# Performance work log

Measured on AMD Instinct MI355X. Metric: run time of the kernel, lower is better.

The kernel has to match this reference:

```python
import jax, jax.numpy as jnp
import numpy as np

NEG_INF = -9e15  # matches torch's -9000000000000000.0 fill
ALPHA = 0.2      # LeakyReLU negative slope


def setup_inputs() -> dict:
    key = jax.random.key(0)
    k1, k2, k3, k4 = jax.random.split(key, 4)
    B, F, N, T, C = 16, 128, 256, 64, 64
    h = jax.random.normal(k1, (B, F, N, T), dtype=jnp.float32)
    adj = jax.random.randint(k2, (B, N, N), 0, 2, dtype=jnp.int32)
    W = jax.random.normal(k3, (B, F, C), dtype=jnp.float32)
    a = jax.random.normal(k4, (B, 2 * C, 1), dtype=jnp.float32)
    return {"h": h, "adj": adj, "W": W, "a": a}


def reference(h, adj, W, a):
    # Wh: (B, C, N, T)
    Wh = jnp.einsum('bfnt,bfc->bcnt', h, W)
    C = W.shape[-1]
    # The original builds the O(N^2) pairwise concat then contracts with a.
    # Equivalently: e[b,i,j,t] = leakyrelu(a1.Wh[:, i] + a2.Wh[:, j])
    a1 = a[:, :C, 0]   # (B, C)
    a2 = a[:, C:, 0]   # (B, C)
    f = jnp.einsum('bcnt,bc->bnt', Wh, a1)  # (B, N, T)
    g = jnp.einsum('bcnt,bc->bnt', Wh, a2)  # (B, N, T)
    e = jax.nn.leaky_relu(f[:, :, None, :] + g[:, None, :, :], negative_slope=ALPHA)  # (B,N,N,T)
    mask = adj[:, :, :, None] > 0  # (B, N, N, 1) broadcast over T
    e = jnp.where(mask, e, NEG_INF)
    attention = jax.nn.softmax(e, axis=2)  # softmax over neighbor index m
    # dropout = 0.0 (eval-mode reference), so skipped
    h_prime = jnp.einsum('bnmt,bcmt->bcnt', attention, Wh)
    return jax.nn.elu(h_prime)  # concat=True branch
```

## Files before the change

### kernel.cpp

```cpp
#include <hip/hip_runtime.h>

#define B_ 16
#define F_ 128
#define N_ 256
#define T_ 64
#define C_ 64
#define ALPHA_ 0.2f
#define L2E_ 1.4426950408889634f

typedef short bf16x8 __attribute__((ext_vector_type(8)));
typedef float f32x4 __attribute__((ext_vector_type(4)));

__device__ __forceinline__ unsigned short f2bf(float x){
  unsigned int u = __float_as_uint(x);
  unsigned int r = u + 0x7FFFu + ((u >> 16) & 1u);
  return (unsigned short)(r >> 16);
}
__device__ __forceinline__ unsigned pk2(float a, float b){
  return ((unsigned)f2bf(b) << 16) | (unsigned)f2bf(a);
}
__device__ __forceinline__ unsigned sbit(unsigned w, int j){
  return (unsigned)(((int)(w << (31 - j))) >> 31);
}
__device__ __forceinline__ int swzT(int c){
  return ((c & 7) ^ ((c >> 3) & 7)) << 4;
}

__global__ void k_u(const float* __restrict__ W, const float* __restrict__ a,
                    float* __restrict__ u){
  int b = blockIdx.x, f = threadIdx.x;
  const float* Wb = W + (b*F_ + f)*C_;
  const float* ab = a + b*2*C_;
  float s1 = 0.f, s2 = 0.f;
#pragma unroll 8
  for (int c = 0; c < C_; ++c){
    float w = Wb[c];
    s1 = fmaf(w, ab[c], s1);
    s2 = fmaf(w, ab[C_ + c], s2);
  }
  u[b*F_ + f] = s1;
  u[B_*F_ + b*F_ + f] = s2;
}

__global__ __launch_bounds__(256, 4) void k_whm(const float* __restrict__ h,
    const float* __restrict__ W, const float* __restrict__ u,
    const int* __restrict__ adj,
    unsigned short* __restrict__ wht, float* __restrict__ fvec,
    float* __restrict__ gvec, unsigned* __restrict__ amask){
  __shared__ uint4 hT4[1024];
  __shared__ uint4 wT4[1024];
  __shared__ float fpart[4][T_];
  __shared__ float gpart[4][T_];
  char* hT = (char*)hT4;
  char* wT = (char*)wT4;

  int bid = blockIdx.x;
  int tid = threadIdx.x, w = tid >> 6, l = tid & 63;

  if (bid >= B_*N_){
    int blk = bid - B_*N_;
    int b = blk >> 2, r0 = (blk & 3)*64;
    const int* ab = adj + ((size_t)b*N_ + r0 + w*16)*N_;
    unsigned* om = amask + ((size_t)b*N_ + r0 + w*16)*8;
    for (int r = 0; r < 16; ++r){
      unsigned long long m0 = __ballot(ab[r*N_ +       l] > 0);
      unsigned long long m1 = __ballot(ab[r*N_ +  64 + l] > 0);
      unsigned long long m2 = __ballot(ab[r*N_ + 128 + l] > 0);
      unsigned long long m3 = __ballot(ab[r*N_ + 192 + l] > 0);
      if (l == 0){
        *(uint4*)(om + r*8)     = make_uint4((unsigned)m0, (unsigned)(m0>>32),
                                             (unsigned)m1, (unsigned)(m1>>32));
        *(uint4*)(om + r*8 + 4) = make_uint4((unsigned)m2, (unsigned)(m2>>32),
                                             (unsigned)m3, (unsigned)(m3>>32));
      }
    }
    return;
  }

  int b = bid >> 8, n = bid & 255;
  const float* hg = h + (size_t)b*F_*N_*T_ + n*T_;
  const float* Wg = W + b*F_*C_;
  const float* u1 = u + b*F_;
  const float* u2 = u + B_*F_ + b*F_;

  float sf = 0.f, sg = 0.f;
#pragma unroll
  for (int p = 0; p < 4; ++p){
    int f0 = p*32 + w*8;
    float v[8], wv[8];
#pragma unroll
    for (int j = 0; j < 8; ++j){
      v[j]  = hg[(size_t)(f0+j)*(N_*T_) + l];
      wv[j] = Wg[(f0+j)*C_ + l];
      sf = fmaf(v[j], u1[f0+j], sf);
      sg = fmaf(v[j], u2[f0+j], sg);
    }
    uint4 ph = make_uint4(pk2(v[0],v[1]),  pk2(v[2],v[3]),  pk2(v[4],v[5]),  pk2(v[6],v[7]));
    uint4 pw = make_uint4(pk2(wv[0],wv[1]),pk2(wv[2],wv[3]),pk2(wv[4],wv[5]),pk2(wv[6],wv[7]));
    *(uint4*)(hT + ((l*256 + f0*2) ^ ((l & 7) << 4))) = ph;
    *(uint4*)(wT + ((l*256 + f0*2) ^ ((l & 7) << 4))) = pw;
  }
  fpart[w][l] = sf;
  gpart[w][l] = sg;
  __syncthreads();

  if (tid < T_){
    float f_ = (fpart[0][tid] + fpart[1][tid]) + (fpart[2][tid] + fpart[3][tid]);
    float g_ = (gpart[0][tid] + gpart[1][tid]) + (gpart[2][tid] + gpart[3][tid]);
    fvec[(b*N_ + n)*T_ + tid] = f_ * L2E_;
    gvec[(b*N_ + n)*T_ + tid] = g_ * L2E_;
  }

  int li = l & 15, g_ = l >> 4;
  bf16x8 afr[4];
#pragma unroll
  for (int ch = 0; ch < 4; ++ch){
    int c = w*16 + li;
    afr[ch] = *(bf16x8*)(wT + ((c*256 + (ch*32 + g_*8)*2) ^ ((c & 7) << 4)));
  }
  f32x4 acc[4];
#pragma unroll
  for (int tt = 0; tt < 4; ++tt) acc[tt] = (f32x4){0.f,0.f,0.f,0.f};
#pragma unroll
  for (int tt = 0; tt < 4; ++tt){
#pragma unroll
    for (int ch = 0; ch < 4; ++ch){
      int t = tt*16 + li;
      bf16x8 bfr = *(bf16x8*)(hT + ((t*256 + (ch*32 + g_*8)*2) ^ ((t & 7) << 4)));
      acc[tt] = __builtin_amdgcn_mfma_f32_16x16x32_bf16(afr[ch], bfr, acc[tt], 0, 0, 0);
    }
  }

  __syncthreads();
  char* outT = hT;
#pragma unroll
  for (int tt = 0; tt < 4; ++tt){
    int t = tt*16 + li;
    int c0 = w*16 + g_*4;
    unsigned q0 = pk2(acc[tt][0], acc[tt][1]);
    unsigned q1 = pk2(acc[tt][2], acc[tt][3]);
    *(uint2*)(outT + ((t*128 + c0*2) ^ ((t & 7) << 4))) = make_uint2(q0, q1);
  }
  __syncthreads();
  unsigned short* wb = wht + (size_t)b*T_*N_*C_ + n*C_;
#pragma unroll
  for (int k = 0; k < 2; ++k){
    int idx = tid + k*256;
    int t = idx >> 3, c8 = idx & 7;
    uint4 vq = *(const uint4*)(outT + t*128 + ((c8 ^ (t & 7)) << 4));
    *(uint4*)(wb + (size_t)t*(N_*C_) + c8*8) = vq;
  }
}

__global__ __launch_bounds__(256, 4) void k_attn(
    unsigned short* wht,
    const unsigned* __restrict__ amask,
    const float* __restrict__ fvec,
    const float* __restrict__ gvec){
  __shared__ uint4 whsT4[2048];
  __shared__ float gs[N_];
  __shared__ float fs[N_];
  __shared__ float invs[N_];
  char* dstT = (char*)whsT4;

  int bid = blockIdx.x;
  int b = bid >> 6, t = bid & 63;
  int tid = threadIdx.x, w = tid >> 6, l = tid & 63;
  int li = l & 15, g_ = l >> 4;

  gs[tid] = gvec[(b*N_ + tid)*T_ + t];
  fs[tid] = fvec[(b*N_ + tid)*T_ + t];

  uint4 mlo[4], mhi[4];
#pragma unroll
  for (int mt = 0; mt < 4; ++mt){
    int n = w*64 + mt*16 + li;
    const uint4* mp = (const uint4*)(amask + ((size_t)b*N_ + n)*8);
    mlo[mt] = mp[0];
    mhi[mt] = mp[1];
  }
  unsigned pkl[4], pkh[4];
  unsigned selA = 0x0C0C0000u | ((unsigned)(g_ + 4) << 8) | (unsigned)g_;
#pragma unroll
  for (int mt = 0; mt < 4; ++mt){
    unsigned t0 = __builtin_amdgcn_perm(mlo[mt].y, mlo[mt].x, selA);
    unsigned t1 = __builtin_amdgcn_perm(mlo[mt].w, mlo[mt].z, selA);
    pkl[mt] = __builtin_amdgcn_perm(t1, t0, 0x05040100u);
    unsigned t2 = __builtin_amdgcn_perm(mhi[mt].y, mhi[mt].x, selA);
    unsigned t3 = __builtin_amdgcn_perm(mhi[mt].w, mhi[mt].z, selA);
    pkh[mt] = __builtin_amdgcn_perm(t3, t2, 0x05040100u);
  }

  const char* src = (const char*)(wht + (size_t)(b*T_ + t)*(N_*C_));
  uint4 ra[4], rb[4];
#pragma unroll
  for (int i = 0; i < 4; ++i){
    int q2 = tid + i*256;
    int m = (q2 >> 3)*2, c0 = (q2 & 7)*8;
    ra[i] = *(const uint4*)(src + m*128 + c0*2);
    rb[i] = *(const uint4*)(src + (m+1)*128 + c0*2);
  }

  asm volatile("s_waitcnt lgkmcnt(0)" ::: "memory");
  __builtin_amdgcn_sched_barrier(0);
  __builtin_amdgcn_s_barrier();

  float fl2[4];
#pragma unroll
  for (int mt = 0; mt < 4; ++mt) fl2[mt] = fs[w*64 + mt*16 + li];

  float mg[4] = {0.f, 0.f, 0.f, 0.f};
#pragma unroll 1
  for (int ch = 0; ch < 8; ++ch){
    const float* gq = &gs[ch*32 + g_*8];
    float4 ga = *(const float4*)gq;
    float4 gb = *(const float4*)(gq + 4);
    float gg[8] = {ga.x, ga.y, ga.z, ga.w, gb.x, gb.y, gb.z, gb.w};
    int sh = (ch & 3)*8;
#pragma unroll
    for (int mt = 0; mt < 4; ++mt){
      unsigned wsh = ((ch & 4) ? pkh[mt] : pkl[mt]) >> sh;
      float cd[8];
#pragma unroll
      for (int j = 0; j < 8; ++j)
        cd[j] = __uint_as_float(__float_as_uint(gg[j]) & sbit(wsh, j));
      float m01 = fmaxf(cd[0], cd[1]), m23 = fmaxf(cd[2], cd[3]);
      float m45 = fmaxf(cd[4], cd[5]), m67 = fmaxf(cd[6], cd[7]);
      mg[mt] = fmaxf(mg[mt], fmaxf(fmaxf(m01, m23), fmaxf(m45, m67)));
    }
  }
  float fme[4], fme2[4];
#pragma unroll
  for (int mt = 0; mt < 4; ++mt){
    float v = mg[mt];
    v = fmaxf(v, __shfl_xor(v, 16));
    v = fmaxf(v, __shfl_xor(v, 32));
    float em = fl2[mt] + v;
    float M  = fmaxf(em, ALPHA_*em);
    fme[mt]  = fl2[mt] - M;
    fme2[mt] = fmaf(fl2[mt], ALPHA_, -M);
  }

#pragma unroll
  for (int i = 0; i < 4; ++i){
    int q2 = tid + i*256;
    int m = (q2 >> 3)*2, c0 = (q2 & 7)*8;
    unsigned va[4] = {ra[i].x, ra[i].y, ra[i].z, ra[i].w};
    unsigned vb[4] = {rb[i].x, rb[i].y, rb[i].z, rb[i].w};
#pragma unroll
    for (int k = 0; k < 4; ++k){
      int c = c0 + 2*k;
      unsigned lo = __builtin_amdgcn_perm(vb[k], va[k], 0x05040100u);
      unsigned hi = __builtin_amdgcn_perm(vb[k], va[k], 0x07060302u);
      *(unsigned*)(dstT + ((c*512 + m*2)     ^ swzT(c)))   = lo;
      *(unsigned*)(dstT + (((c+1)*512 + m*2) ^ swzT(c+1))) = hi;
    }
  }
  __syncthreads();

  f32x4 acc[4][4];
#pragma unroll
  for (int mt = 0; mt < 4; ++mt)
#pragma unroll
    for (int nt = 0; nt < 4; ++nt)
      acc[mt][nt] = (f32x4){0.f, 0.f, 0.f, 0.f};
  float s0[4] = {0.f,0.f,0.f,0.f}, s1[4] = {0.f,0.f,0.f,0.f};

#pragma unroll 2
  for (int ch = 0; ch < 8; ++ch){
    bf16x8 bfr[4];
#pragma unroll
    for (int nt = 0; nt < 4; ++nt){
      int c = nt*16 + li;
      bfr[nt] = *(bf16x8*)(dstT + ((c*512 + (ch*32 + g_*8)*2) ^ swzT(c)));
    }
    const float* gq = &gs[ch*32 + g_*8];
    float4 ga = *(const float4*)gq;
    float4 gb = *(const float4*)(gq + 4);
    float gg[8] = {ga.x, ga.y, ga.z, ga.w, gb.x, gb.y, gb.z, gb.w};
    int sh = (ch & 3)*8;
#pragma unroll
    for (int mt = 0; mt < 4; ++mt){
      unsigned wsh = ((ch & 4) ? pkh[mt] : pkl[mt]) >> sh;
      float wv[8];
#pragma unroll
      for (int j = 0; j < 8; ++j){
        float d1 = gg[j] + fme[mt];
        float d2 = fmaf(gg[j], ALPHA_, fme2[mt]);
        float p  = exp2f(fmaxf(d1, d2));
        float v  = __uint_as_float(__float_as_uint(p) & sbit(wsh, j));
        if (j < 4) s0[mt] += v; else s1[mt] += v;
        wv[j] = v;
      }
      unsigned q0, q1, q2_, q3;
      asm("v_cvt_pk_bf16_f32 %0, %1, %2" : "=v"(q0)  : "v"(wv[0]), "v"(wv[1]));
      asm("v_cvt_pk_bf16_f32 %0, %1, %2" : "=v"(q1)  : "v"(wv[2]), "v"(wv[3]));
      asm("v_cvt_pk_bf16_f32 %0, %1, %2" : "=v"(q2_) : "v"(wv[4]), "v"(wv[5]));
      asm("v_cvt_pk_bf16_f32 %0, %1, %2" : "=v"(q3)  : "v"(wv[6]), "v"(wv[7]));
      union { unsigned u[4]; bf16x8 v; } afu;
      afu.u[0] = q0; afu.u[1] = q1; afu.u[2] = q2_; afu.u[3] = q3;
#pragma unroll
      for (int nt = 0; nt < 4; ++nt)
        acc[mt][nt] = __builtin_amdgcn_mfma_f32_16x16x32_bf16(afu.v, bfr[nt], acc[mt][nt], 0, 0, 0);
    }
  }

#pragma unroll
  for (int mt = 0; mt < 4; ++mt){
    float s = s0[mt] + s1[mt];
    s += __shfl_xor(s, 16);
    s += __shfl_xor(s, 32);
    if (g_ == 0) invs[w*64 + mt*16 + li] = 1.0f / s;
  }

  unsigned short* ob = wht + (size_t)(b*T_ + t)*(N_*C_);
#pragma unroll
  for (int mt = 0; mt < 4; ++mt){
#pragma unroll
    for (int reg = 0; reg < 4; ++reg){
      int nloc = w*64 + mt*16 + g_*4 + reg;
      float inv = invs[nloc];
#pragma unroll
      for (int nt = 0; nt < 4; ++nt){
        float v = acc[mt][nt][reg] * inv;
        v = v > 0.f ? v : (__expf(v) - 1.f);
        ob[nloc*C_ + nt*16 + li] = f2bf(v);
      }
    }
  }
}

__global__ __launch_bounds__(256) void k_tr(const unsigned short* __restrict__ whtO,
                                            float* __restrict__ out){
  __shared__ float tile[64][65];
  int bid = blockIdx.x;
  int b = bid >> 8, n = bid & 255;
  int tid = threadIdx.x;
  const unsigned short* src = whtO + ((size_t)b*T_*N_ + n)*C_;
#pragma unroll
  for (int i = 0; i < 2; ++i){
    int idx = tid + i*256;
    int t = idx >> 3, c0 = (idx & 7)*8;
    uint4 v = *(const uint4*)(src + (size_t)t*(N_*C_) + c0);
    unsigned arr[4] = {v.x, v.y, v.z, v.w};
#pragma unroll
    for (int k = 0; k < 4; ++k){
      tile[c0+2*k  ][t] = __uint_as_float(arr[k] << 16);
      tile[c0+2*k+1][t] = __uint_as_float(arr[k] & 0xFFFF0000u);
    }
  }
  __syncthreads();
  float* ob = out + (size_t)b*C_*N_*T_ + n*T_;
#pragma unroll
  for (int i = 0; i < 4; ++i){
    int idx = tid + i*256;
    int c = idx >> 4, t0 = (idx & 15)*4;
    float4 v = make_float4(tile[c][t0], tile[c][t0+1], tile[c][t0+2], tile[c][t0+3]);
    *(float4*)(ob + (size_t)c*(N_*T_) + t0) = v;
  }
}

extern "C" void kernel_launch(void* const* d_in, const int* in_sizes, int n_in,
                              void* d_out, int out_size, void* d_ws, size_t ws_size,
                              hipStream_t stream){
  (void)in_sizes; (void)n_in; (void)out_size; (void)ws_size;
  const float* h   = (const float*)d_in[0];
  const int*   adj = (const int*)d_in[1];
  const float* W   = (const float*)d_in[2];
  const float* a   = (const float*)d_in[3];
  float* u    = (float*)d_ws;
  float* fvec = u + 2*B_*F_;
  float* gvec = fvec + B_*N_*T_;
  unsigned short* wht = (unsigned short*)(gvec + B_*N_*T_);
  unsigned* amask = (unsigned*)(wht + (size_t)B_*T_*N_*C_);

  k_u   <<<dim3(B_),           dim3(F_),  0, stream>>>(W, a, u);
  k_whm <<<dim3(B_*N_ + B_*4), dim3(256), 0, stream>>>(h, W, u, adj, wht, fvec, gvec, amask);
  k_attn<<<dim3(B_*T_),        dim3(256), 0, stream>>>(wht, amask, fvec, gvec);
  k_tr  <<<dim3(B_*N_),        dim3(256), 0, stream>>>(wht, (float*)d_out);
}
```

Baseline: 105.5 us.

## Split attention kernel over two row halves per (batch, time) block

Each k_attn block now handles 128 of the 256 query rows instead of all of them, which doubles the grid to 2048 blocks and halves per-thread accumulators. The output goes to a separate workspace buffer, because the in-place write would race with the other half-block still reading the same Wh slice. The aim is more blocks and less register pressure for better occupancy and load balance. In exchange, every block still loads and transposes the full Wh tile into LDS, so that staging work is duplicated.

New measurement: 103.1 us, median of 2. 1.02x faster.

```diff
diff --git a/kernel.cpp b/kernel.cpp
--- a/kernel.cpp
+++ b/kernel.cpp
@@ -153,36 +153,38 @@
 }
 
 __global__ __launch_bounds__(256, 4) void k_attn(
-    unsigned short* wht,
+    const unsigned short* __restrict__ wht,
+    unsigned short* __restrict__ wout,
     const unsigned* __restrict__ amask,
     const float* __restrict__ fvec,
     const float* __restrict__ gvec){
   __shared__ uint4 whsT4[2048];
   __shared__ float gs[N_];
-  __shared__ float fs[N_];
-  __shared__ float invs[N_];
+  __shared__ float fs[128];
+  __shared__ float invs[128];
   char* dstT = (char*)whsT4;
 
   int bid = blockIdx.x;
-  int b = bid >> 6, t = bid & 63;
+  int b = bid >> 7, t = (bid >> 1) & 63, nh = bid & 1;
+  int nbase = nh*128;
   int tid = threadIdx.x, w = tid >> 6, l = tid & 63;
   int li = l & 15, g_ = l >> 4;
 
   gs[tid] = gvec[(b*N_ + tid)*T_ + t];
-  fs[tid] = fvec[(b*N_ + tid)*T_ + t];
-
-  uint4 mlo[4], mhi[4];
-#pragma unroll
-  for (int mt = 0; mt < 4; ++mt){
-    int n = w*64 + mt*16 + li;
+  if (tid < 128) fs[tid] = fvec[(b*N_ + nbase + tid)*T_ + t];
+
+  uint4 mlo[2], mhi[2];
+#pragma unroll
+  for (int mt = 0; mt < 2; ++mt){
+    int n = nbase + w*32 + mt*16 + li;
     const uint4* mp = (const uint4*)(amask + ((size_t)b*N_ + n)*8);
     mlo[mt] = mp[0];
     mhi[mt] = mp[1];
   }
-  unsigned pkl[4], pkh[4];
+  unsigned pkl[2], pkh[2];
   unsigned selA = 0x0C0C0000u | ((unsigned)(g_ + 4) << 8) | (unsigned)g_;
 #pragma unroll
-  for (int mt = 0; mt < 4; ++mt){
+  for (int mt = 0; mt < 2; ++mt){
     unsigned t0 = __builtin_amdgcn_perm(mlo[mt].y, mlo[mt].x, selA);
     unsigned t1 = __builtin_amdgcn_perm(mlo[mt].w, mlo[mt].z, selA);
     pkl[mt] = __builtin_amdgcn_perm(t1, t0, 0x05040100u);
@@ -205,11 +207,11 @@
   __builtin_amdgcn_sched_barrier(0);
   __builtin_amdgcn_s_barrier();
 
-  float fl2[4];
-#pragma unroll
-  for (int mt = 0; mt < 4; ++mt) fl2[mt] = fs[w*64 + mt*16 + li];
-
-  float mg[4] = {0.f, 0.f, 0.f, 0.f};
+  float fl2[2];
+#pragma unroll
+  for (int mt = 0; mt < 2; ++mt) fl2[mt] = fs[w*32 + mt*16 + li];
+
+  float mg[2] = {0.f, 0.f};
 #pragma unroll 1
   for (int ch = 0; ch < 8; ++ch){
     const float* gq = &gs[ch*32 + g_*8];
@@ -218,7 +220,7 @@
     float gg[8] = {ga.x, ga.y, ga.z, ga.w, gb.x, gb.y, gb.z, gb.w};
     int sh = (ch & 3)*8;
 #pragma unroll
-    for (int mt = 0; mt < 4; ++mt){
+    for (int mt = 0; mt < 2; ++mt){
       unsigned wsh = ((ch & 4) ? pkh[mt] : pkl[mt]) >> sh;
       float cd[8];
 #pragma unroll
@@ -229,9 +231,9 @@
       mg[mt] = fmaxf(mg[mt], fmaxf(fmaxf(m01, m23), fmaxf(m45, m67)));
     }
   }
-  float fme[4], fme2[4];
-#pragma unroll
-  for (int mt = 0; mt < 4; ++mt){
+  float fme[2], fme2[2];
+#pragma unroll
+  for (int mt = 0; mt < 2; ++mt){
     float v = mg[mt];
     v = fmaxf(v, __shfl_xor(v, 16));
     v = fmaxf(v, __shfl_xor(v, 32));
@@ -258,13 +260,13 @@
   }
   __syncthreads();
 
-  f32x4 acc[4][4];
-#pragma unroll
-  for (int mt = 0; mt < 4; ++mt)
+  f32x4 acc[2][4];
+#pragma unroll
+  for (int mt = 0; mt < 2; ++mt)
 #pragma unroll
     for (int nt = 0; nt < 4; ++nt)
       acc[mt][nt] = (f32x4){0.f, 0.f, 0.f, 0.f};
-  float s0[4] = {0.f,0.f,0.f,0.f}, s1[4] = {0.f,0.f,0.f,0.f};
+  float s0[2] = {0.f,0.f}, s1[2] = {0.f,0.f};
 
 #pragma unroll 2
   for (int ch = 0; ch < 8; ++ch){
@@ -280,7 +282,7 @@
     float gg[8] = {ga.x, ga.y, ga.z, ga.w, gb.x, gb.y, gb.z, gb.w};
     int sh = (ch & 3)*8;
 #pragma unroll
-    for (int mt = 0; mt < 4; ++mt){
+    for (int mt = 0; mt < 2; ++mt){
       unsigned wsh = ((ch & 4) ? pkh[mt] : pkl[mt]) >> sh;
       float wv[8];
 #pragma unroll
@@ -306,25 +308,25 @@
   }
 
 #pragma unroll
-  for (int mt = 0; mt < 4; ++mt){
+  for (int mt = 0; mt < 2; ++mt){
     float s = s0[mt] + s1[mt];
     s += __shfl_xor(s, 16);
     s += __shfl_xor(s, 32);
-    if (g_ == 0) invs[w*64 + mt*16 + li] = 1.0f / s;
-  }
-
-  unsigned short* ob = wht + (size_t)(b*T_ + t)*(N_*C_);
-#pragma unroll
-  for (int mt = 0; mt < 4; ++mt){
+    if (g_ == 0) invs[w*32 + mt*16 + li] = 1.0f / s;
+  }
+
+  unsigned short* ob = wout + (size_t)(b*T_ + t)*(N_*C_) + (size_t)nbase*C_;
+#pragma unroll
+  for (int mt = 0; mt < 2; ++mt){
 #pragma unroll
     for (int reg = 0; reg < 4; ++reg){
-      int nloc = w*64 + mt*16 + g_*4 + reg;
-      float inv = invs[nloc];
+      int rloc = w*32 + mt*16 + g_*4 + reg;
+      float inv = invs[rloc];
 #pragma unroll
       for (int nt = 0; nt < 4; ++nt){
         float v = acc[mt][nt][reg] * inv;
         v = v > 0.f ? v : (__expf(v) - 1.f);
-        ob[nloc*C_ + nt*16 + li] = f2bf(v);
+        ob[rloc*C_ + nt*16 + li] = f2bf(v);
       }
     }
   }
@@ -373,9 +375,10 @@
   float* gvec = fvec + B_*N_*T_;
   unsigned short* wht = (unsigned short*)(gvec + B_*N_*T_);
   unsigned* amask = (unsigned*)(wht + (size_t)B_*T_*N_*C_);
+  unsigned short* wout = (unsigned short*)(amask + (size_t)B_*N_*8);
 
   k_u   <<<dim3(B_),           dim3(F_),  0, stream>>>(W, a, u);
   k_whm <<<dim3(B_*N_ + B_*4), dim3(256), 0, stream>>>(h, W, u, adj, wht, fvec, gvec, amask);
-  k_attn<<<dim3(B_*T_),        dim3(256), 0, stream>>>(wht, amask, fvec, gvec);
-  k_tr  <<<dim3(B_*N_),        dim3(256), 0, stream>>>(wht, (float*)d_out);
-}
+  k_attn<<<dim3(B_*T_*2),      dim3(256), 0, stream>>>(wht, wout, amask, fvec, gvec);
+  k_tr  <<<dim3(B_*N_),        dim3(256), 0, stream>>>(wout, (float*)d_out);
+}
```
